# Optimization experiments

Hardware: AMD Instinct MI355X
Metric: run time of the kernel (lower is better)

## Reference

```python
import jax, jax.numpy as jnp
import numpy as np

N_NODES = 50000
N_EDGES = 800000
IN_CH = 128
OUT_CH = 64
HEADS = 2
NEG_SLOPE = 0.2


def _gat_conv(x, src, dst, W, a_src, a_dst, b, n):
    """PyG-style GATConv (eval mode: no dropout), self-loops already appended.
    x: [n, F_in]; W: [F_in, H*C]; a_src/a_dst: [H, C]; b: [H*C]."""
    H, C = a_src.shape
    h = (x @ W).reshape(n, H, C)                       # [n, H, C]
    alpha_src = jnp.sum(h * a_src, axis=-1)            # [n, H]
    alpha_dst = jnp.sum(h * a_dst, axis=-1)            # [n, H]
    e = alpha_src[src] + alpha_dst[dst]                # [E, H]
    e = jnp.where(e > 0, e, NEG_SLOPE * e)             # LeakyReLU(0.2)
    # neighbor-wise (destination-grouped) softmax, numerically stable
    m = jax.ops.segment_max(e, dst, num_segments=n)
    e = jnp.exp(e - m[dst])
    denom = jax.ops.segment_sum(e, dst, num_segments=n)
    alpha = e / (denom[dst] + 1e-16)                   # [E, H]
    out = jax.ops.segment_sum(alpha[:, :, None] * h[src], dst, num_segments=n)
    return out.reshape(n, H * C) + b


def setup_inputs() -> dict:
    key = jax.random.key(0)
    ks = jax.random.split(key, 12)
    s = 0.08  # glorot-ish scale
    x = jax.random.normal(ks[0], (N_NODES, IN_CH), dtype=jnp.float32)
    edge_index = jax.random.randint(ks[1], (2, N_EDGES), 0, N_NODES, dtype=jnp.int64)
    H, O = HEADS, OUT_CH
    return {
        "x": x,
        "edge_index": edge_index,
        "W1": jax.random.normal(ks[2], (IN_CH, H * 2 * O), dtype=jnp.float32) * s,
        "a_src1": jax.random.normal(ks[3], (H, 2 * O), dtype=jnp.float32) * s,
        "a_dst1": jax.random.normal(ks[4], (H, 2 * O), dtype=jnp.float32) * s,
        "b1": jnp.zeros((H * 2 * O,), dtype=jnp.float32),
        "W_mu": jax.random.normal(ks[5], (2 * O * H, H * O), dtype=jnp.float32) * s,
        "a_src_mu": jax.random.normal(ks[6], (H, O), dtype=jnp.float32) * s,
        "a_dst_mu": jax.random.normal(ks[7], (H, O), dtype=jnp.float32) * s,
        "b_mu": jnp.zeros((H * O,), dtype=jnp.float32),
        "W_ls": jax.random.normal(ks[8], (2 * O * H, H * O), dtype=jnp.float32) * s,
        "a_src_ls": jax.random.normal(ks[9], (H, O), dtype=jnp.float32) * s,
        "a_dst_ls": jax.random.normal(ks[10], (H, O), dtype=jnp.float32) * s,
        "b_ls": jnp.zeros((H * O,), dtype=jnp.float32),
    }


def reference(x, edge_index, W1, a_src1, a_dst1, b1,
              W_mu, a_src_mu, a_dst_mu, b_mu,
              W_ls, a_src_ls, a_dst_ls, b_ls):
    n = x.shape[0]
    loop = jnp.arange(n, dtype=edge_index.dtype)
    src = jnp.concatenate([edge_index[0], loop])  # PyG add_self_loops=True
    dst = jnp.concatenate([edge_index[1], loop])
    x1 = jax.nn.elu(_gat_conv(x, src, dst, W1, a_src1, a_dst1, b1, n))
    mu = _gat_conv(x1, src, dst, W_mu, a_src_mu, a_dst_mu, b_mu, n)
    logstd = _gat_conv(x1, src, dst, W_ls, a_src_ls, a_dst_ls, b_ls, n)
    return (mu, logstd)
```

## Files before the change

kernel.cpp:

```cpp
#include <hip/hip_runtime.h>


typedef unsigned short u16;
typedef unsigned int u32;
typedef _Float16 f16;
typedef f16 f16x8 __attribute__((ext_vector_type(8)));
typedef float f32x4v __attribute__((ext_vector_type(4)));

__device__ __forceinline__ u16 f2h(float f) {
    union { f16 h; u16 u; } t;
    t.h = (f16)f;
    return t.u;
}
__device__ __forceinline__ float4 loadh4(const u16* __restrict__ p, size_t i) {
    union { uint2 u; f16 h[4]; } t;
    t.u = *(const uint2*)(p + i);
    return make_float4((float)t.h[0], (float)t.h[1], (float)t.h[2], (float)t.h[3]);
}
__device__ __forceinline__ void store4(float* __restrict__ p, size_t i, float4 v) {
    *(float4*)(p + i) = v;
}
__device__ __forceinline__ void store4(u16* __restrict__ p, size_t i, float4 v) {
    union { uint2 u; f16 h[4]; } t;
    t.h[0] = (f16)v.x; t.h[1] = (f16)v.y; t.h[2] = (f16)v.z; t.h[3] = (f16)v.w;
    *(uint2*)(p + i) = t.u;
}

__global__ __launch_bounds__(256) void k_detect(const u32* __restrict__ ebuf,
                                                int* __restrict__ flag) {
    __shared__ int nz;
    if (threadIdx.x == 0) nz = 0;
    __syncthreads();
    if (ebuf[2 * threadIdx.x + 1] != 0u) atomicAdd(&nz, 1);
    __syncthreads();
    if (threadIdx.x == 0) *flag = (nz == 0) ? 1 : 0;
}

__global__ __launch_bounds__(256) void k_extract(const u32* __restrict__ ebuf, int E,
                                                 const int* __restrict__ flag,
                                                 int* __restrict__ se,
                                                 int* __restrict__ de,
                                                 int* __restrict__ deg) {
    int e = blockIdx.x * 256 + threadIdx.x;
    if (e >= E) return;
    int s, d;
    if (*flag) {
        s = (int)ebuf[2 * (size_t)e];
        d = (int)ebuf[2 * ((size_t)E + (size_t)e)];
    } else {
        s = (int)ebuf[e];
        d = (int)ebuf[(size_t)E + (size_t)e];
    }
    se[e] = s;
    de[e] = d;
    atomicAdd(&deg[d], 1);
}

__global__ __launch_bounds__(256) void k_scan_a(const int* __restrict__ deg, int n,
                                                int* __restrict__ bsum) {
    __shared__ int s[256];
    int i = blockIdx.x * 256 + threadIdx.x;
    s[threadIdx.x] = (i < n) ? deg[i] : 0;
    __syncthreads();
    for (int st = 128; st > 0; st >>= 1) {
        if (threadIdx.x < st) s[threadIdx.x] += s[threadIdx.x + st];
        __syncthreads();
    }
    if (threadIdx.x == 0) bsum[blockIdx.x] = s[0];
}

__global__ __launch_bounds__(256) void k_scan_b(int* __restrict__ bsum, int nb) {
    __shared__ int s[256];
    int t = threadIdx.x;
    int v = (t < nb) ? bsum[t] : 0;
    s[t] = v;
    __syncthreads();
    for (int off = 1; off < 256; off <<= 1) {
        int add = (t >= off) ? s[t - off] : 0;
        __syncthreads();
        s[t] += add;
        __syncthreads();
    }
    if (t < nb) bsum[t] = s[t] - v;
}

__global__ __launch_bounds__(256) void k_scan_c(const int* __restrict__ deg, int n,
                                                const int* __restrict__ bsum,
                                                int* __restrict__ rowptr,
                                                int* __restrict__ cursor, int E) {
    __shared__ int s[256];
    int t = threadIdx.x;
    int i = blockIdx.x * 256 + t;
    int v = (i < n) ? deg[i] : 0;
    s[t] = v;
    __syncthreads();
    for (int off = 1; off < 256; off <<= 1) {
        int add = (t >= off) ? s[t - off] : 0;
        __syncthreads();
        s[t] += add;
        __syncthreads();
    }
    if (i < n) {
        int ex = bsum[blockIdx.x] + s[t] - v;
        rowptr[i] = ex;
        cursor[i] = ex;
    }
    if (i == 0) rowptr[n] = E;
}

__global__ __launch_bounds__(256) void k_fill(const int* __restrict__ src,
                                              const int* __restrict__ dst, int E,
                                              int* __restrict__ cursor,
                                              int* __restrict__ csr_src,
                                              int* __restrict__ csr_dst) {
    int e = blockIdx.x * 256 + threadIdx.x;
    if (e < E) {
        int d = dst[e];
        int slot = atomicAdd(&cursor[d], 1);
        csr_src[slot] = src[e];
        csr_dst[slot] = d;
    }
}

__global__ __launch_bounds__(256) void k_tw(const float* __restrict__ Wl,
                                            const float* __restrict__ Wr, int split,
                                            int K, u16* __restrict__ Wt) {
    int idx = blockIdx.x * 256 + threadIdx.x;
    if (idx >= 256 * K) return;
    int c = idx / K, k = idx - c * K;
    float v;
    if (split == 256)
        v = Wl[(size_t)k * 256 + c];
    else
        v = (c < 128) ? Wl[(size_t)k * 128 + c] : Wr[(size_t)k * 128 + (c - 128)];
    Wt[idx] = f2h(v);
}

template <int NS>
__global__ __launch_bounds__(256) void k_w(const int* __restrict__ csr_src,
                                           const int* __restrict__ csr_dst,
                                           const float* __restrict__ as,
                                           const float* __restrict__ ad,
                                           float* __restrict__ wp, int E) {
    int i = blockIdx.x * 256 + threadIdx.x;
    if (i >= E) return;
    int s = csr_src[i], d = csr_dst[i];
    if (NS == 2) {
        float2 a = *(const float2*)(as + (size_t)s * 2);
        float2 b = *(const float2*)(ad + (size_t)d * 2);
        float e0 = a.x + b.x, e1 = a.y + b.y;
        e0 = fmaxf(e0, 0.2f * e0);
        e1 = fmaxf(e1, 0.2f * e1);
        wp[i] = __expf(e0);
        wp[(size_t)E + i] = __expf(e1);
    } else {
        float4 a = *(const float4*)(as + (size_t)s * 4);
        float4 b = *(const float4*)(ad + (size_t)d * 4);
        float e0 = a.x + b.x, e1 = a.y + b.y, e2 = a.z + b.z, e3 = a.w + b.w;
        e0 = fmaxf(e0, 0.2f * e0);
        e1 = fmaxf(e1, 0.2f * e1);
        e2 = fmaxf(e2, 0.2f * e2);
        e3 = fmaxf(e3, 0.2f * e3);
        wp[i] = __expf(e0);
        wp[(size_t)E + i] = __expf(e1);
        wp[2 * (size_t)E + i] = __expf(e2);
        wp[3 * (size_t)E + i] = __expf(e3);
    }
}

template <int K, int ALOGW, bool AF32>
__global__ __launch_bounds__(256) void k_gemm_mfma(
    const void* __restrict__ Av, const u16* __restrict__ Wt, u16* __restrict__ out,
    float* __restrict__ as_out, float* __restrict__ ad_out,
    const float* __restrict__ alo, const float* __restrict__ ahi,
    const float* __restrict__ dlo, const float* __restrict__ dhi, int M) {
    __shared__ u16 Bs[256 * 40];
    const int tid = threadIdx.x;
    const int wave = tid >> 6;
    const int lane = tid & 63;
    const int li = lane & 15;
    const int quad = lane >> 4;
    const int r0 = blockIdx.x * 128 + wave * 32;
    int ar0 = r0 + li;
    int ar1 = r0 + 16 + li;
    if (ar0 >= M) ar0 = M - 1;
    if (ar1 >= M) ar1 = M - 1;
    const u16* a16_0 = (const u16*)Av + (size_t)ar0 * K + quad * 8;
    const u16* a16_1 = (const u16*)Av + (size_t)ar1 * K + quad * 8;
    const float* a32_0 = (const float*)Av + (size_t)ar0 * K + quad * 8;
    const float* a32_1 = (const float*)Av + (size_t)ar1 * K + quad * 8;

    f32x4v acc0[16], acc1[16];
#pragma unroll
    for (int ct = 0; ct < 16; ct++) {
        acc0[ct] = (f32x4v)(0.f);
        acc1[ct] = (f32x4v)(0.f);
    }

    const u16* wrow = Wt + (size_t)tid * K;
    u16* dstp = Bs + tid * 40;
    uint4 sv0 = ((const uint4*)wrow)[0];
    uint4 sv1 = ((const uint4*)(wrow + 8))[0];
    uint4 sv2 = ((const uint4*)(wrow + 16))[0];
    uint4 sv3 = ((const uint4*)(wrow + 24))[0];
    uint4 p0a, p0b, p1a, p1b;
    if (AF32) {
        p0a = *(const uint4*)(a32_0);
        p0b = *(const uint4*)(a32_0 + 4);
        p1a = *(const uint4*)(a32_1);
        p1b = *(const uint4*)(a32_1 + 4);
    } else {
        p0a = *(const uint4*)(a16_0);
        p1a = *(const uint4*)(a16_1);
        p0b = p0a;
        p1b = p1a;
    }

    for (int t = 0; t < K; t += 32) {
        asm volatile("s_waitcnt lgkmcnt(0)" ::: "memory");
        __builtin_amdgcn_s_barrier();
        ((uint4*)dstp)[0] = sv0;
        ((uint4*)(dstp + 8))[0] = sv1;
        ((uint4*)(dstp + 16))[0] = sv2;
        ((uint4*)(dstp + 24))[0] = sv3;
        f16x8 a0, a1;
        if (AF32) {
            union { uint4 u; float f[4]; } ua, ub;
            ua.u = p0a; ub.u = p0b;
            a0[0] = (f16)ua.f[0]; a0[1] = (f16)ua.f[1];
            a0[2] = (f16)ua.f[2]; a0[3] = (f16)ua.f[3];
            a0[4] = (f16)ub.f[0]; a0[5] = (f16)ub.f[1];
            a0[6] = (f16)ub.f[2]; a0[7] = (f16)ub.f[3];
            ua.u = p1a; ub.u = p1b;
            a1[0] = (f16)ua.f[0]; a1[1] = (f16)ua.f[1];
            a1[2] = (f16)ua.f[2]; a1[3] = (f16)ua.f[3];
            a1[4] = (f16)ub.f[0]; a1[5] = (f16)ub.f[1];
            a1[6] = (f16)ub.f[2]; a1[7] = (f16)ub.f[3];
        } else {
            union { uint4 u; f16x8 h; } uh;
            uh.u = p0a; a0 = uh.h;
            uh.u = p1a; a1 = uh.h;
        }
        if (t + 32 < K) {
            const u16* s2 = wrow + t + 32;
            sv0 = ((const uint4*)s2)[0];
            sv1 = ((const uint4*)(s2 + 8))[0];
            sv2 = ((const uint4*)(s2 + 16))[0];
            sv3 = ((const uint4*)(s2 + 24))[0];
            if (AF32) {
                p0a = *(const uint4*)(a32_0 + t + 32);
                p0b = *(const uint4*)(a32_0 + t + 36);
                p1a = *(const uint4*)(a32_1 + t + 32);
                p1b = *(const uint4*)(a32_1 + t + 36);
            } else {
                p0a = *(const uint4*)(a16_0 + t + 32);
                p1a = *(const uint4*)(a16_1 + t + 32);
            }
        }
        asm volatile("s_waitcnt lgkmcnt(0)" ::: "memory");
        __builtin_amdgcn_s_barrier();
#pragma unroll
        for (int ct = 0; ct < 16; ct++) {
            f16x8 b = *(const f16x8*)(Bs + (ct * 16 + li) * 40 + quad * 8);
            acc0[ct] = __builtin_amdgcn_mfma_f32_16x16x32_f16(a0, b, acc0[ct], 0, 0, 0);
            acc1[ct] = __builtin_amdgcn_mfma_f32_16x16x32_f16(a1, b, acc1[ct], 0, 0, 0);
        }
    }

    const int NS = 64 >> ALOGW;
    const int SH = ALOGW - 2;
    float aw[16], dw[16];
#pragma unroll
    for (int ct = 0; ct < 16; ct++) {
        int col = ct * 16 + li;
        aw[ct] = (col < 128) ? alo[col] : ahi[col - 128];
        dw[ct] = (col < 128) ? dlo[col] : dhi[col - 128];
    }

    auto epilogue = [&](f32x4v(&acc)[16], int rbase) {
#pragma unroll
        for (int reg = 0; reg < 4; reg++) {
            int grow = rbase + quad * 4 + reg;
            if (grow < M) {
                u16* orow = out + (size_t)grow * 256 + li;
#pragma unroll
                for (int ct = 0; ct < 16; ct++) orow[ct * 16] = f2h(acc[ct][reg]);
            }
        }
#pragma unroll
        for (int reg = 0; reg < 4; reg++) {
            float s[4] = {0.f, 0.f, 0.f, 0.f};
            float d[4] = {0.f, 0.f, 0.f, 0.f};
#pragma unroll
            for (int ct = 0; ct < 16; ct++) {
                int sl = ct >> SH;
                s[sl] += acc[ct][reg] * aw[ct];
                d[sl] += acc[ct][reg] * dw[ct];
            }
#pragma unroll
            for (int sl = 0; sl < NS; sl++) {
#pragma unroll
                for (int m = 1; m <= 8; m <<= 1) {
                    s[sl] += __shfl_xor(s[sl], m, 64);
                    d[sl] += __shfl_xor(d[sl], m, 64);
                }
            }
            int grow = rbase + quad * 4 + reg;
            if (li == 0 && grow < M) {
#pragma unroll
                for (int sl = 0; sl < NS; sl++) {
                    as_out[(size_t)grow * NS + sl] = s[sl];
                    ad_out[(size_t)grow * NS + sl] = d[sl];
                }
            }
        }
    };
    epilogue(acc0, r0);
    epilogue(acc1, r0 + 16);
}

template <int LOGW, int MODE, typename OT>
__global__ __launch_bounds__(256) void k_agg4(
    const u16* __restrict__ h, const int* __restrict__ rowptr,
    const int* __restrict__ csr_src, const float* __restrict__ wp,
    const float* __restrict__ as, const float* __restrict__ ad,
    const float* __restrict__ b_lo, const float* __restrict__ b_hi,
    OT* __restrict__ outp, int n, int nGrp, int E) {
    const int NS = 64 >> LOGW;
    const int bid = blockIdx.x;
    const int xcd = bid & 7;
    const int half = xcd >> 2;
    const int grp = (bid >> 3) * 4 + (xcd & 3);
    if (grp >= nGrp) return;
    const int lane = threadIdx.x & 63;
    const int sub = lane >> 5;
    const int sl = lane & 31;
    const int wid0 = grp * 8 + (threadIdx.x >> 6) * 2 + sub;
    const bool ok = wid0 < n;
    const int wid = ok ? wid0 : (n - 1);
    const int col = half * 128 + sl * 4;
    const int slot = col >> (LOGW + 2);
    const float* __restrict__ wpl = wp + (size_t)slot * E;

    float e = as[(size_t)wid * NS + slot] + ad[(size_t)wid * NS + slot];
    e = fmaxf(e, 0.2f * e);
    float w = __expf(e);
    float denom = w;
    float4 hv = loadh4(h, (size_t)wid * 256 + col);
    float acc0 = w * hv.x, acc1 = w * hv.y, acc2 = w * hv.z, acc3 = w * hv.w;

    int rb = 0, re = 0;
    if (ok) { rb = rowptr[wid0]; re = rowptr[wid0 + 1]; }
    int p = rb;
    for (; p + 8 <= re; p += 8) {
        int4 sA = *(const int4*)(csr_src + p);
        int4 sB = *(const int4*)(csr_src + p + 4);
        float4 wA = *(const float4*)(wpl + p);
        float4 wB = *(const float4*)(wpl + p + 4);
        float4 h0 = loadh4(h, (size_t)sA.x * 256 + col);
        float4 h1 = loadh4(h, (size_t)sA.y * 256 + col);
        float4 h2 = loadh4(h, (size_t)sA.z * 256 + col);
        float4 h3 = loadh4(h, (size_t)sA.w * 256 + col);
        float4 h4 = loadh4(h, (size_t)sB.x * 256 + col);
        float4 h5 = loadh4(h, (size_t)sB.y * 256 + col);
        float4 h6 = loadh4(h, (size_t)sB.z * 256 + col);
        float4 h7 = loadh4(h, (size_t)sB.w * 256 + col);
        denom += (wA.x + wA.y + wA.z + wA.w) + (wB.x + wB.y + wB.z + wB.w);
        acc0 += wA.x * h0.x + wA.y * h1.x + wA.z * h2.x + wA.w * h3.x +
                wB.x * h4.x + wB.y * h5.x + wB.z * h6.x + wB.w * h7.x;
        acc1 += wA.x * h0.y + wA.y * h1.y + wA.z * h2.y + wA.w * h3.y +
                wB.x * h4.y + wB.y * h5.y + wB.z * h6.y + wB.w * h7.y;
        acc2 += wA.x * h0.z + wA.y * h1.z + wA.z * h2.z + wA.w * h3.z +
                wB.x * h4.z + wB.y * h5.z + wB.z * h6.z + wB.w * h7.z;
        acc3 += wA.x * h0.w + wA.y * h1.w + wA.z * h2.w + wA.w * h3.w +
                wB.x * h4.w + wB.y * h5.w + wB.z * h6.w + wB.w * h7.w;
    }
    for (; p + 4 <= re; p += 4) {
        int4 sA = *(const int4*)(csr_src + p);
        float4 wA = *(const float4*)(wpl + p);
        float4 h0 = loadh4(h, (size_t)sA.x * 256 + col);
        float4 h1 = loadh4(h, (size_t)sA.y * 256 + col);
        float4 h2 = loadh4(h, (size_t)sA.z * 256 + col);
        float4 h3 = loadh4(h, (size_t)sA.w * 256 + col);
        denom += (wA.x + wA.y) + (wA.z + wA.w);
        acc0 += wA.x * h0.x + wA.y * h1.x + wA.z * h2.x + wA.w * h3.x;
        acc1 += wA.x * h0.y + wA.y * h1.y + wA.z * h2.y + wA.w * h3.y;
        acc2 += wA.x * h0.z + wA.y * h1.z + wA.z * h2.z + wA.w * h3.z;
        acc3 += wA.x * h0.w + wA.y * h1.w + wA.z * h2.w + wA.w * h3.w;
    }
    for (; p < re; ++p) {
        int s = csr_src[p];
        float ww = wpl[p];
        float4 hh = loadh4(h, (size_t)s * 256 + col);
        denom += ww;
        acc0 += ww * hh.x;
        acc1 += ww * hh.y;
        acc2 += ww * hh.z;
        acc3 += ww * hh.w;
    }
    float inv = 1.0f / (denom + 1e-16f);

    const float* bp = half ? b_hi : b_lo;
    const int ci = sl * 4;
    float4 bv = *(const float4*)(bp + ci);
    float v0 = acc0 * inv + bv.x;
    float v1 = acc1 * inv + bv.y;
    float v2 = acc2 * inv + bv.z;
    float v3 = acc3 * inv + bv.w;

    if (!ok) return;
    if (MODE == 0) {
        v0 = v0 > 0.f ? v0 : expm1f(v0);
        v1 = v1 > 0.f ? v1 : expm1f(v1);
        v2 = v2 > 0.f ? v2 : expm1f(v2);
        v3 = v3 > 0.f ? v3 : expm1f(v3);
        store4((u16*)outp, (size_t)wid0 * 256 + col, make_float4(v0, v1, v2, v3));
    } else {
        size_t base = half ? ((size_t)n * 128 + (size_t)wid0 * 128 + ci)
                           : ((size_t)wid0 * 128 + ci);
        store4((float*)outp, base, make_float4(v0, v1, v2, v3));
    }
}

extern "C" void kernel_launch(void* const* d_in, const int* in_sizes, int n_in,
                              void* d_out, int out_size, void* d_ws, size_t ws_size,
                              hipStream_t stream) {
    const float* x = (const float*)d_in[0];
    const u32* ebuf = (const u32*)d_in[1];
    const float* W1 = (const float*)d_in[2];
    const float* a_src1 = (const float*)d_in[3];
    const float* a_dst1 = (const float*)d_in[4];
    const float* b1 = (const float*)d_in[5];
    const float* W_mu = (const float*)d_in[6];
    const float* a_src_mu = (const float*)d_in[7];
    const float* a_dst_mu = (const float*)d_in[8];
    const float* b_mu = (const float*)d_in[9];
    const float* W_ls = (const float*)d_in[10];
    const float* a_src_ls = (const float*)d_in[11];
    const float* a_dst_ls = (const float*)d_in[12];
    const float* b_ls = (const float*)d_in[13];

    const int n = in_sizes[0] / 128;
    const int E = in_sizes[1] / 2;

    char* base = (char*)d_ws;
    size_t off = 0;
    auto alloc = [&](size_t b) -> char* {
        char* p = base + off;
        off = (off + b + 255) & ~(size_t)255;
        return p;
    };
    int* rowptr = (int*)alloc((size_t)(n + 1) * 4);
    int* cursor = (int*)alloc((size_t)n * 4);
    int* csr = (int*)alloc((size_t)E * 4);
    int* csrd = (int*)alloc((size_t)E * 4);
    int* bsum = (int*)alloc(256 * 4);
    int* eflag = (int*)alloc(256);
    int* se = (int*)alloc((size_t)E * 4);
    int* de = (int*)alloc((size_t)E * 4);
    float* as = (float*)alloc((size_t)n * 4 * 4);
    float* ad = (float*)alloc((size_t)n * 4 * 4);
    float* wp = (float*)alloc((size_t)E * 4 * 4);
    u16* W1t = (u16*)alloc(256 * 128 * 2);
    u16* Wt2 = (u16*)alloc(256 * 256 * 2);
    u16* x1h = (u16*)alloc((size_t)n * 256 * 2);
    u16* h = (u16*)alloc((size_t)n * 256 * 2);

    const int nb = (n + 255) / 256;
    const int eg = (E + 255) / 256;
    const int gg = (n + 127) / 128;
    const int nGrp = (n + 7) / 8;
    const int aggGrid = 8 * ((nGrp + 3) / 4);

    hipMemsetAsync(cursor, 0, (size_t)n * 4, stream);
    k_detect<<<1, 256, 0, stream>>>(ebuf, eflag);
    k_extract<<<eg, 256, 0, stream>>>(ebuf, E, eflag, se, de, cursor);
    k_scan_a<<<nb, 256, 0, stream>>>(cursor, n, bsum);
    k_scan_b<<<1, 256, 0, stream>>>(bsum, nb);
    k_scan_c<<<nb, 256, 0, stream>>>(cursor, n, bsum, rowptr, cursor, E);
    k_fill<<<eg, 256, 0, stream>>>(se, de, E, cursor, csr, csrd);

    k_tw<<<(256 * 128 + 255) / 256, 256, 0, stream>>>(W1, W1, 256, 128, W1t);
    k_tw<<<(256 * 256 + 255) / 256, 256, 0, stream>>>(W_mu, W_ls, 128, 256, Wt2);

    k_gemm_mfma<128, 5, true><<<gg, 256, 0, stream>>>(x, W1t, h, as, ad, a_src1,
                                                      a_src1 + 128, a_dst1,
                                                      a_dst1 + 128, n);
    k_w<2><<<eg, 256, 0, stream>>>(csr, csrd, as, ad, wp, E);
    k_agg4<5, 0, u16><<<aggGrid, 256, 0, stream>>>(h, rowptr, csr, wp, as, ad, b1,
                                                   b1 + 128, x1h, n, nGrp, E);

    k_gemm_mfma<256, 4, false><<<gg, 256, 0, stream>>>(x1h, Wt2, h, as, ad,
                                                       a_src_mu, a_src_ls,
                                                       a_dst_mu, a_dst_ls, n);
    k_w<4><<<eg, 256, 0, stream>>>(csr, csrd, as, ad, wp, E);
    k_agg4<4, 1, float><<<aggGrid, 256, 0, stream>>>(h, rowptr, csr, wp, as, ad,
                                                     b_mu, b_ls, (float*)d_out, n,
                                                     nGrp, E);
}
```

Measured before the change: 388.4 us.

## Aggregate raw features before layer-1 GEMM and precompute attention vectors

Layer 1 now uses linearity: attention logits come from x·(W·a) vectors computed up front, and neighbour aggregation runs on the 128-wide fp16 input features (per head) before the GEMM with W1. The layer-1 GEMM then applies bias and ELU and produces the layer-2 attention scores from precomputed W_mu/W_ls·a vectors. The separate detect kernel is folded into extract, and edge arrays are padded. The aim is to gather narrower rows in the first aggregation and shrink epilogue work. The cost is a few extra small kernels and a different rounding order for the fp16 aggregates.

After: 432.2 us. 11.3% more time.

```diff
diff --git a/kernel.cpp b/kernel.cpp
--- a/kernel.cpp
+++ b/kernel.cpp
@@ -20,31 +20,26 @@
 __device__ __forceinline__ void store4(float* __restrict__ p, size_t i, float4 v) {
     *(float4*)(p + i) = v;
 }
-__device__ __forceinline__ void store4(u16* __restrict__ p, size_t i, float4 v) {
+__device__ __forceinline__ void store4h(u16* __restrict__ p, size_t i, float4 v) {
     union { uint2 u; f16 h[4]; } t;
     t.h[0] = (f16)v.x; t.h[1] = (f16)v.y; t.h[2] = (f16)v.z; t.h[3] = (f16)v.w;
     *(uint2*)(p + i) = t.u;
 }
 
-__global__ __launch_bounds__(256) void k_detect(const u32* __restrict__ ebuf,
-                                                int* __restrict__ flag) {
+__global__ __launch_bounds__(256) void k_extract(const u32* __restrict__ ebuf, int E,
+                                                 int* __restrict__ se,
+                                                 int* __restrict__ de,
+                                                 int* __restrict__ deg) {
     __shared__ int nz;
     if (threadIdx.x == 0) nz = 0;
     __syncthreads();
     if (ebuf[2 * threadIdx.x + 1] != 0u) atomicAdd(&nz, 1);
     __syncthreads();
-    if (threadIdx.x == 0) *flag = (nz == 0) ? 1 : 0;
-}
-
-__global__ __launch_bounds__(256) void k_extract(const u32* __restrict__ ebuf, int E,
-                                                 const int* __restrict__ flag,
-                                                 int* __restrict__ se,
-                                                 int* __restrict__ de,
-                                                 int* __restrict__ deg) {
+    const bool i64 = (nz == 0);
     int e = blockIdx.x * 256 + threadIdx.x;
     if (e >= E) return;
     int s, d;
-    if (*flag) {
+    if (i64) {
         s = (int)ebuf[2 * (size_t)e];
         d = (int)ebuf[2 * ((size_t)E + (size_t)e)];
     } else {
@@ -114,6 +109,7 @@
                                               int* __restrict__ csr_src,
                                               int* __restrict__ csr_dst) {
     int e = blockIdx.x * 256 + threadIdx.x;
+    if (e < 8) csr_src[E + e] = 0;
     if (e < E) {
         int d = dst[e];
         int slot = atomicAdd(&cursor[d], 1);
@@ -136,12 +132,89 @@
     Wt[idx] = f2h(v);
 }
 
+__global__ void k_vdots1(const float* __restrict__ W1,
+                         const float* __restrict__ a_src,
+                         const float* __restrict__ a_dst,
+                         float* __restrict__ v1) {
+    int c = threadIdx.x;
+    if (c >= 128) return;
+    const float* wr = W1 + (size_t)c * 256;
+    float s0 = 0, s1 = 0, d0 = 0, d1 = 0;
+    for (int j = 0; j < 128; j++) {
+        float w0 = wr[j], w1 = wr[128 + j];
+        s0 += w0 * a_src[j];
+        s1 += w1 * a_src[128 + j];
+        d0 += w0 * a_dst[j];
+        d1 += w1 * a_dst[128 + j];
+    }
+    v1[c] = s0;
+    v1[128 + c] = s1;
+    v1[256 + c] = d0;
+    v1[384 + c] = d1;
+}
+
+__global__ void k_vdots2(const float* __restrict__ Wmu, const float* __restrict__ Wls,
+                         const float* __restrict__ smu, const float* __restrict__ dmu,
+                         const float* __restrict__ sls, const float* __restrict__ dls,
+                         float* __restrict__ v2s, float* __restrict__ v2d) {
+    int j = threadIdx.x;
+    const float* wm = Wmu + (size_t)j * 128;
+    const float* wl = Wls + (size_t)j * 128;
+    float s0 = 0, s1 = 0, s2 = 0, s3 = 0, d0 = 0, d1 = 0, d2 = 0, d3 = 0;
+    for (int k = 0; k < 64; k++) {
+        float m0 = wm[k], m1 = wm[64 + k], l0 = wl[k], l1 = wl[64 + k];
+        s0 += m0 * smu[k];
+        s1 += m1 * smu[64 + k];
+        s2 += l0 * sls[k];
+        s3 += l1 * sls[64 + k];
+        d0 += m0 * dmu[k];
+        d1 += m1 * dmu[64 + k];
+        d2 += l0 * dls[k];
+        d3 += l1 * dls[64 + k];
+    }
+    v2s[j] = s0; v2s[256 + j] = s1; v2s[512 + j] = s2; v2s[768 + j] = s3;
+    v2d[j] = d0; v2d[256 + j] = d1; v2d[512 + j] = d2; v2d[768 + j] = d3;
+}
+
+__global__ __launch_bounds__(256) void k_cvt_asad(const float* __restrict__ x,
+                                                  const float* __restrict__ v1,
+                                                  u16* __restrict__ xh,
+                                                  float* __restrict__ as,
+                                                  float* __restrict__ ad, int n) {
+    int wid = blockIdx.x * 4 + (threadIdx.x >> 6);
+    if (wid >= n) return;
+    int lane = threadIdx.x & 63;
+    float2 xv = *(const float2*)(x + (size_t)wid * 128 + lane * 2);
+    union { u32 u; f16 h[2]; } t;
+    t.h[0] = (f16)xv.x;
+    t.h[1] = (f16)xv.y;
+    *(u32*)(xh + (size_t)wid * 128 + lane * 2) = t.u;
+    int c = lane * 2;
+    float s0 = xv.x * v1[c] + xv.y * v1[c + 1];
+    float s1 = xv.x * v1[128 + c] + xv.y * v1[128 + c + 1];
+    float d0 = xv.x * v1[256 + c] + xv.y * v1[256 + c + 1];
+    float d1 = xv.x * v1[384 + c] + xv.y * v1[384 + c + 1];
+#pragma unroll
+    for (int m = 1; m <= 32; m <<= 1) {
+        s0 += __shfl_xor(s0, m, 64);
+        s1 += __shfl_xor(s1, m, 64);
+        d0 += __shfl_xor(d0, m, 64);
+        d1 += __shfl_xor(d1, m, 64);
+    }
+    if (lane == 0) {
+        as[(size_t)wid * 2] = s0;
+        as[(size_t)wid * 2 + 1] = s1;
+        ad[(size_t)wid * 2] = d0;
+        ad[(size_t)wid * 2 + 1] = d1;
+    }
+}
+
 template <int NS>
 __global__ __launch_bounds__(256) void k_w(const int* __restrict__ csr_src,
                                            const int* __restrict__ csr_dst,
                                            const float* __restrict__ as,
                                            const float* __restrict__ ad,
-                                           float* __restrict__ wp, int E) {
+                                           float* __restrict__ wp, int E, int Ep) {
     int i = blockIdx.x * 256 + threadIdx.x;
     if (i >= E) return;
     int s = csr_src[i], d = csr_dst[i];
@@ -152,7 +225,7 @@
         e0 = fmaxf(e0, 0.2f * e0);
         e1 = fmaxf(e1, 0.2f * e1);
         wp[i] = __expf(e0);
-        wp[(size_t)E + i] = __expf(e1);
+        wp[(size_t)Ep + i] = __expf(e1);
     } else {
         float4 a = *(const float4*)(as + (size_t)s * 4);
         float4 b = *(const float4*)(ad + (size_t)d * 4);
@@ -162,18 +235,116 @@
         e2 = fmaxf(e2, 0.2f * e2);
         e3 = fmaxf(e3, 0.2f * e3);
         wp[i] = __expf(e0);
-        wp[(size_t)E + i] = __expf(e1);
-        wp[2 * (size_t)E + i] = __expf(e2);
-        wp[3 * (size_t)E + i] = __expf(e3);
-    }
-}
-
-template <int K, int ALOGW, bool AF32>
-__global__ __launch_bounds__(256) void k_gemm_mfma(
-    const void* __restrict__ Av, const u16* __restrict__ Wt, u16* __restrict__ out,
+        wp[(size_t)Ep + i] = __expf(e1);
+        wp[2 * (size_t)Ep + i] = __expf(e2);
+        wp[3 * (size_t)Ep + i] = __expf(e3);
+    }
+}
+
+__global__ __launch_bounds__(256) void k_agg1(
+    const u16* __restrict__ xh, const int* __restrict__ rowptr,
+    const int* __restrict__ csr_src, const float* __restrict__ wp,
+    const float* __restrict__ as, const float* __restrict__ ad,
+    u16* __restrict__ aggout, int n, int Ep) {
+    const int lane = threadIdx.x & 63;
+    const int sub = lane >> 5;
+    const int sl = lane & 31;
+    const int wid0 = blockIdx.x * 8 + (threadIdx.x >> 6) * 2 + sub;
+    const bool ok = wid0 < n;
+    const int wid = ok ? wid0 : (n - 1);
+    const int col = sl * 4;
+    const float* __restrict__ wp0 = wp;
+    const float* __restrict__ wp1 = wp + Ep;
+
+    float e0 = as[(size_t)wid * 2] + ad[(size_t)wid * 2];
+    float e1 = as[(size_t)wid * 2 + 1] + ad[(size_t)wid * 2 + 1];
+    e0 = fmaxf(e0, 0.2f * e0);
+    e1 = fmaxf(e1, 0.2f * e1);
+    float w0s = __expf(e0), w1s = __expf(e1);
+    float den0 = w0s, den1 = w1s;
+    float4 hv = loadh4(xh, (size_t)wid * 128 + col);
+    float a0x = w0s * hv.x, a0y = w0s * hv.y, a0z = w0s * hv.z, a0w = w0s * hv.w;
+    float b0x = w1s * hv.x, b0y = w1s * hv.y, b0z = w1s * hv.z, b0w = w1s * hv.w;
+
+    int rb = 0, re = 0;
+    if (ok) { rb = rowptr[wid0]; re = rowptr[wid0 + 1]; }
+    int p = rb;
+    for (; p + 8 <= re; p += 8) {
+        int4 sA = *(const int4*)(csr_src + p);
+        int4 sB = *(const int4*)(csr_src + p + 4);
+        float4 uA = *(const float4*)(wp0 + p);
+        float4 uB = *(const float4*)(wp0 + p + 4);
+        float4 vA = *(const float4*)(wp1 + p);
+        float4 vB = *(const float4*)(wp1 + p + 4);
+        float4 h0 = loadh4(xh, (size_t)sA.x * 128 + col);
+        float4 h1 = loadh4(xh, (size_t)sA.y * 128 + col);
+        float4 h2 = loadh4(xh, (size_t)sA.z * 128 + col);
+        float4 h3 = loadh4(xh, (size_t)sA.w * 128 + col);
+        float4 h4 = loadh4(xh, (size_t)sB.x * 128 + col);
+        float4 h5 = loadh4(xh, (size_t)sB.y * 128 + col);
+        float4 h6 = loadh4(xh, (size_t)sB.z * 128 + col);
+        float4 h7 = loadh4(xh, (size_t)sB.w * 128 + col);
+        den0 += (uA.x + uA.y + uA.z + uA.w) + (uB.x + uB.y + uB.z + uB.w);
+        den1 += (vA.x + vA.y + vA.z + vA.w) + (vB.x + vB.y + vB.z + vB.w);
+        a0x += uA.x * h0.x + uA.y * h1.x + uA.z * h2.x + uA.w * h3.x +
+               uB.x * h4.x + uB.y * h5.x + uB.z * h6.x + uB.w * h7.x;
+        a0y += uA.x * h0.y + uA.y * h1.y + uA.z * h2.y + uA.w * h3.y +
+               uB.x * h4.y + uB.y * h5.y + uB.z * h6.y + uB.w * h7.y;
+        a0z += uA.x * h0.z + uA.y * h1.z + uA.z * h2.z + uA.w * h3.z +
+               uB.x * h4.z + uB.y * h5.z + uB.z * h6.z + uB.w * h7.z;
+        a0w += uA.x * h0.w + uA.y * h1.w + uA.z * h2.w + uA.w * h3.w +
+               uB.x * h4.w + uB.y * h5.w + uB.z * h6.w + uB.w * h7.w;
+        b0x += vA.x * h0.x + vA.y * h1.x + vA.z * h2.x + vA.w * h3.x +
+               vB.x * h4.x + vB.y * h5.x + vB.z * h6.x + vB.w * h7.x;
+        b0y += vA.x * h0.y + vA.y * h1.y + vA.z * h2.y + vA.w * h3.y +
+               vB.x * h4.y + vB.y * h5.y + vB.z * h6.y + vB.w * h7.y;
+        b0z += vA.x * h0.z + vA.y * h1.z + vA.z * h2.z + vA.w * h3.z +
+               vB.x * h4.z + vB.y * h5.z + vB.z * h6.z + vB.w * h7.z;
+        b0w += vA.x * h0.w + vA.y * h1.w + vA.z * h2.w + vA.w * h3.w +
+               vB.x * h4.w + vB.y * h5.w + vB.z * h6.w + vB.w * h7.w;
+    }
+    for (; p + 4 <= re; p += 4) {
+        int4 sA = *(const int4*)(csr_src + p);
+        float4 uA = *(const float4*)(wp0 + p);
+        float4 vA = *(const float4*)(wp1 + p);
+        float4 h0 = loadh4(xh, (size_t)sA.x * 128 + col);
+        float4 h1 = loadh4(xh, (size_t)sA.y * 128 + col);
+        float4 h2 = loadh4(xh, (size_t)sA.z * 128 + col);
+        float4 h3 = loadh4(xh, (size_t)sA.w * 128 + col);
+        den0 += (uA.x + uA.y) + (uA.z + uA.w);
+        den1 += (vA.x + vA.y) + (vA.z + vA.w);
+        a0x += uA.x * h0.x + uA.y * h1.x + uA.z * h2.x + uA.w * h3.x;
+        a0y += uA.x * h0.y + uA.y * h1.y + uA.z * h2.y + uA.w * h3.y;
+        a0z += uA.x * h0.z + uA.y * h1.z + uA.z * h2.z + uA.w * h3.z;
+        a0w += uA.x * h0.w + uA.y * h1.w + uA.z * h2.w + uA.w * h3.w;
+        b0x += vA.x * h0.x + vA.y * h1.x + vA.z * h2.x + vA.w * h3.x;
+        b0y += vA.x * h0.y + vA.y * h1.y + vA.z * h2.y + vA.w * h3.y;
+        b0z += vA.x * h0.z + vA.y * h1.z + vA.z * h2.z + vA.w * h3.z;
+        b0w += vA.x * h0.w + vA.y * h1.w + vA.z * h2.w + vA.w * h3.w;
+    }
+    for (; p < re; ++p) {
+        int s = csr_src[p];
+        float u = wp0[p], v = wp1[p];
+        float4 hh = loadh4(xh, (size_t)s * 128 + col);
+        den0 += u;
+        den1 += v;
+        a0x += u * hh.x; a0y += u * hh.y; a0z += u * hh.z; a0w += u * hh.w;
+        b0x += v * hh.x; b0y += v * hh.y; b0z += v * hh.z; b0w += v * hh.w;
+    }
+    if (!ok) return;
+    float i0 = 1.0f / (den0 + 1e-16f);
+    float i1 = 1.0f / (den1 + 1e-16f);
+    store4h(aggout, (size_t)wid0 * 256 + col,
+            make_float4(a0x * i0, a0y * i0, a0z * i0, a0w * i0));
+    store4h(aggout, (size_t)wid0 * 256 + 128 + col,
+            make_float4(b0x * i1, b0y * i1, b0z * i1, b0w * i1));
+}
+
+__global__ __launch_bounds__(256) void k_gemm_x1(
+    const u16* __restrict__ Ag, const u16* __restrict__ Wt, u16* __restrict__ x1out,
     float* __restrict__ as_out, float* __restrict__ ad_out,
-    const float* __restrict__ alo, const float* __restrict__ ahi,
-    const float* __restrict__ dlo, const float* __restrict__ dhi, int M) {
+    const float* __restrict__ b1, const float* __restrict__ v2s,
+    const float* __restrict__ v2d, int M) {
     __shared__ u16 Bs[256 * 40];
     const int tid = threadIdx.x;
     const int wave = tid >> 6;
@@ -185,10 +356,10 @@
     int ar1 = r0 + 16 + li;
     if (ar0 >= M) ar0 = M - 1;
     if (ar1 >= M) ar1 = M - 1;
-    const u16* a16_0 = (const u16*)Av + (size_t)ar0 * K + quad * 8;
-    const u16* a16_1 = (const u16*)Av + (size_t)ar1 * K + quad * 8;
-    const float* a32_0 = (const float*)Av + (size_t)ar0 * K + quad * 8;
-    const float* a32_1 = (const float*)Av + (size_t)ar1 * K + quad * 8;
+    const u16* a00p = Ag + (size_t)ar0 * 256 + quad * 8;
+    const u16* a01p = Ag + (size_t)ar0 * 256 + 128 + quad * 8;
+    const u16* a10p = Ag + (size_t)ar1 * 256 + quad * 8;
+    const u16* a11p = Ag + (size_t)ar1 * 256 + 128 + quad * 8;
 
     f32x4v acc0[16], acc1[16];
 #pragma unroll
@@ -197,65 +368,163 @@
         acc1[ct] = (f32x4v)(0.f);
     }
 
-    const u16* wrow = Wt + (size_t)tid * K;
+    const u16* wrow = Wt + (size_t)tid * 128;
     u16* dstp = Bs + tid * 40;
     uint4 sv0 = ((const uint4*)wrow)[0];
     uint4 sv1 = ((const uint4*)(wrow + 8))[0];
     uint4 sv2 = ((const uint4*)(wrow + 16))[0];
     uint4 sv3 = ((const uint4*)(wrow + 24))[0];
-    uint4 p0a, p0b, p1a, p1b;
-    if (AF32) {
-        p0a = *(const uint4*)(a32_0);
-        p0b = *(const uint4*)(a32_0 + 4);
-        p1a = *(const uint4*)(a32_1);
-        p1b = *(const uint4*)(a32_1 + 4);
-    } else {
-        p0a = *(const uint4*)(a16_0);
-        p1a = *(const uint4*)(a16_1);
-        p0b = p0a;
-        p1b = p1a;
-    }
-
-    for (int t = 0; t < K; t += 32) {
+    uint4 p00 = *(const uint4*)a00p;
+    uint4 p01 = *(const uint4*)a01p;
+    uint4 p10 = *(const uint4*)a10p;
+    uint4 p11 = *(const uint4*)a11p;
+
+    for (int t = 0; t < 128; t += 32) {
         asm volatile("s_waitcnt lgkmcnt(0)" ::: "memory");
         __builtin_amdgcn_s_barrier();
         ((uint4*)dstp)[0] = sv0;
         ((uint4*)(dstp + 8))[0] = sv1;
         ((uint4*)(dstp + 16))[0] = sv2;
         ((uint4*)(dstp + 24))[0] = sv3;
-        f16x8 a0, a1;
-        if (AF32) {
-            union { uint4 u; float f[4]; } ua, ub;
-            ua.u = p0a; ub.u = p0b;
-            a0[0] = (f16)ua.f[0]; a0[1] = (f16)ua.f[1];
-            a0[2] = (f16)ua.f[2]; a0[3] = (f16)ua.f[3];
-            a0[4] = (f16)ub.f[0]; a0[5] = (f16)ub.f[1];
-            a0[6] = (f16)ub.f[2]; a0[7] = (f16)ub.f[3];
-            ua.u = p1a; ub.u = p1b;
-            a1[0] = (f16)ua.f[0]; a1[1] = (f16)ua.f[1];
-            a1[2] = (f16)ua.f[2]; a1[3] = (f16)ua.f[3];
-            a1[4] = (f16)ub.f[0]; a1[5] = (f16)ub.f[1];
-            a1[6] = (f16)ub.f[2]; a1[7] = (f16)ub.f[3];
-        } else {
-            union { uint4 u; f16x8 h; } uh;
-            uh.u = p0a; a0 = uh.h;
-            uh.u = p1a; a1 = uh.h;
-        }
-        if (t + 32 < K) {
+        union { uint4 u; f16x8 h; } uh;
+        f16x8 a00, a01, a10, a11;
+        uh.u = p00; a00 = uh.h;
+        uh.u = p01; a01 = uh.h;
+        uh.u = p10; a10 = uh.h;
+        uh.u = p11; a11 = uh.h;
+        if (t + 32 < 128) {
             const u16* s2 = wrow + t + 32;
             sv0 = ((const uint4*)s2)[0];
             sv1 = ((const uint4*)(s2 + 8))[0];
             sv2 = ((const uint4*)(s2 + 16))[0];
             sv3 = ((const uint4*)(s2 + 24))[0];
-            if (AF32) {
-                p0a = *(const uint4*)(a32_0 + t + 32);
-                p0b = *(const uint4*)(a32_0 + t + 36);
-                p1a = *(const uint4*)(a32_1 + t + 32);
-                p1b = *(const uint4*)(a32_1 + t + 36);
+            p00 = *(const uint4*)(a00p + t + 32);
+            p01 = *(const uint4*)(a01p + t + 32);
+            p10 = *(const uint4*)(a10p + t + 32);
+            p11 = *(const uint4*)(a11p + t + 32);
+        }
+        asm volatile("s_waitcnt lgkmcnt(0)" ::: "memory");
+        __builtin_amdgcn_s_barrier();
+#pragma unroll
+        for (int ct = 0; ct < 16; ct++) {
+            f16x8 b = *(const f16x8*)(Bs + (ct * 16 + li) * 40 + quad * 8);
+            if (ct < 8) {
+                acc0[ct] = __builtin_amdgcn_mfma_f32_16x16x32_f16(a00, b, acc0[ct], 0, 0, 0);
+                acc1[ct] = __builtin_amdgcn_mfma_f32_16x16x32_f16(a10, b, acc1[ct], 0, 0, 0);
             } else {
-                p0a = *(const uint4*)(a16_0 + t + 32);
-                p1a = *(const uint4*)(a16_1 + t + 32);
+                acc0[ct] = __builtin_amdgcn_mfma_f32_16x16x32_f16(a01, b, acc0[ct], 0, 0, 0);
+                acc1[ct] = __builtin_amdgcn_mfma_f32_16x16x32_f16(a11, b, acc1[ct], 0, 0, 0);
             }
+        }
+    }
+
+    float bval[16];
+#pragma unroll
+    for (int ct = 0; ct < 16; ct++) bval[ct] = b1[ct * 16 + li];
+
+    auto epilogue = [&](f32x4v(&acc)[16], int rbase) {
+#pragma unroll
+        for (int ct = 0; ct < 16; ct++) {
+#pragma unroll
+            for (int reg = 0; reg < 4; reg++) {
+                float v = acc[ct][reg] + bval[ct];
+                acc[ct][reg] = v > 0.f ? v : expm1f(v);
+            }
+        }
+#pragma unroll
+        for (int reg = 0; reg < 4; reg++) {
+            int grow = rbase + quad * 4 + reg;
+            if (grow < M) {
+                u16* orow = x1out + (size_t)grow * 256 + li;
+#pragma unroll
+                for (int ct = 0; ct < 16; ct++) orow[ct * 16] = f2h(acc[ct][reg]);
+            }
+        }
+#pragma unroll
+        for (int sl = 0; sl < 4; sl++) {
+            float aw[16], dw[16];
+#pragma unroll
+            for (int ct = 0; ct < 16; ct++) {
+                aw[ct] = v2s[sl * 256 + ct * 16 + li];
+                dw[ct] = v2d[sl * 256 + ct * 16 + li];
+            }
+#pragma unroll
+            for (int reg = 0; reg < 4; reg++) {
+                float s = 0.f, d = 0.f;
+#pragma unroll
+                for (int ct = 0; ct < 16; ct++) {
+                    s += acc[ct][reg] * aw[ct];
+                    d += acc[ct][reg] * dw[ct];
+                }
+#pragma unroll
+                for (int m = 1; m <= 8; m <<= 1) {
+                    s += __shfl_xor(s, m, 64);
+                    d += __shfl_xor(d, m, 64);
+                }
+                int grow = rbase + quad * 4 + reg;
+                if (li == 0 && grow < M) {
+                    as_out[(size_t)grow * 4 + sl] = s;
+                    ad_out[(size_t)grow * 4 + sl] = d;
+                }
+            }
+        }
+    };
+    epilogue(acc0, r0);
+    epilogue(acc1, r0 + 16);
+}
+
+__global__ __launch_bounds__(256) void k_gemm_h(const u16* __restrict__ Ah,
+                                                const u16* __restrict__ Wt,
+                                                u16* __restrict__ out, int M) {
+    __shared__ u16 Bs[256 * 40];
+    const int tid = threadIdx.x;
+    const int wave = tid >> 6;
+    const int lane = tid & 63;
+    const int li = lane & 15;
+    const int quad = lane >> 4;
+    const int r0 = blockIdx.x * 128 + wave * 32;
+    int ar0 = r0 + li;
+    int ar1 = r0 + 16 + li;
+    if (ar0 >= M) ar0 = M - 1;
+    if (ar1 >= M) ar1 = M - 1;
+    const u16* a0p = Ah + (size_t)ar0 * 256 + quad * 8;
+    const u16* a1p = Ah + (size_t)ar1 * 256 + quad * 8;
+
+    f32x4v acc0[16], acc1[16];
+#pragma unroll
+    for (int ct = 0; ct < 16; ct++) {
+        acc0[ct] = (f32x4v)(0.f);
+        acc1[ct] = (f32x4v)(0.f);
+    }
+
+    const u16* wrow = Wt + (size_t)tid * 256;
+    u16* dstp = Bs + tid * 40;
+    uint4 sv0 = ((const uint4*)wrow)[0];
+    uint4 sv1 = ((const uint4*)(wrow + 8))[0];
+    uint4 sv2 = ((const uint4*)(wrow + 16))[0];
+    uint4 sv3 = ((const uint4*)(wrow + 24))[0];
+    uint4 p0 = *(const uint4*)a0p;
+    uint4 p1 = *(const uint4*)a1p;
+
+    for (int t = 0; t < 256; t += 32) {
+        asm volatile("s_waitcnt lgkmcnt(0)" ::: "memory");
+        __builtin_amdgcn_s_barrier();
+        ((uint4*)dstp)[0] = sv0;
+        ((uint4*)(dstp + 8))[0] = sv1;
+        ((uint4*)(dstp + 16))[0] = sv2;
+        ((uint4*)(dstp + 24))[0] = sv3;
+        union { uint4 u; f16x8 h; } uh;
+        f16x8 a0, a1;
+        uh.u = p0; a0 = uh.h;
+        uh.u = p1; a1 = uh.h;
+        if (t + 32 < 256) {
+            const u16* s2 = wrow + t + 32;
+            sv0 = ((const uint4*)s2)[0];
+            sv1 = ((const uint4*)(s2 + 8))[0];
+            sv2 = ((const uint4*)(s2 + 16))[0];
+            sv3 = ((const uint4*)(s2 + 24))[0];
+            p0 = *(const uint4*)(a0p + t + 32);
+            p1 = *(const uint4*)(a1p + t + 32);
         }
         asm volatile("s_waitcnt lgkmcnt(0)" ::: "memory");
         __builtin_amdgcn_s_barrier();
@@ -266,67 +535,30 @@
             acc1[ct] = __builtin_amdgcn_mfma_f32_16x16x32_f16(a1, b, acc1[ct], 0, 0, 0);
         }
     }
-
-    const int NS = 64 >> ALOGW;
-    const int SH = ALOGW - 2;
-    float aw[16], dw[16];
-#pragma unroll
-    for (int ct = 0; ct < 16; ct++) {
-        int col = ct * 16 + li;
-        aw[ct] = (col < 128) ? alo[col] : ahi[col - 128];
-        dw[ct] = (col < 128) ? dlo[col] : dhi[col - 128];
-    }
-
-    auto epilogue = [&](f32x4v(&acc)[16], int rbase) {
-#pragma unroll
-        for (int reg = 0; reg < 4; reg++) {
-            int grow = rbase + quad * 4 + reg;
-            if (grow < M) {
-                u16* orow = out + (size_t)grow * 256 + li;
-#pragma unroll
-                for (int ct = 0; ct < 16; ct++) orow[ct * 16] = f2h(acc[ct][reg]);
-            }
-        }
-#pragma unroll
-        for (int reg = 0; reg < 4; reg++) {
-            float s[4] = {0.f, 0.f, 0.f, 0.f};
-            float d[4] = {0.f, 0.f, 0.f, 0.f};
-#pragma unroll
-            for (int ct = 0; ct < 16; ct++) {
-                int sl = ct >> SH;
-                s[sl] += acc[ct][reg] * aw[ct];
-                d[sl] += acc[ct][reg] * dw[ct];
-            }
-#pragma unroll
-            for (int sl = 0; sl < NS; sl++) {
-#pragma unroll
-                for (int m = 1; m <= 8; m <<= 1) {
-                    s[sl] += __shfl_xor(s[sl], m, 64);
-                    d[sl] += __shfl_xor(d[sl], m, 64);
-                }
-            }
-            int grow = rbase + quad * 4 + reg;
-            if (li == 0 && grow < M) {
-#pragma unroll
-                for (int sl = 0; sl < NS; sl++) {
-                    as_out[(size_t)grow * NS + sl] = s[sl];
-                    ad_out[(size_t)grow * NS + sl] = d[sl];
-                }
-            }
-        }
-    };
-    epilogue(acc0, r0);
-    epilogue(acc1, r0 + 16);
-}
-
-template <int LOGW, int MODE, typename OT>
+#pragma unroll
+    for (int reg = 0; reg < 4; reg++) {
+        int g0 = r0 + quad * 4 + reg;
+        if (g0 < M) {
+            u16* orow = out + (size_t)g0 * 256 + li;
+#pragma unroll
+            for (int ct = 0; ct < 16; ct++) orow[ct * 16] = f2h(acc0[ct][reg]);
+        }
+        int g1 = r0 + 16 + quad * 4 + reg;
+        if (g1 < M) {
+            u16* orow = out + (size_t)g1 * 256 + li;
+#pragma unroll
+            for (int ct = 0; ct < 16; ct++) orow[ct * 16] = f2h(acc1[ct][reg]);
+        }
+    }
+}
+
 __global__ __launch_bounds__(256) void k_agg4(
     const u16* __restrict__ h, const int* __restrict__ rowptr,
     const int* __restrict__ csr_src, const float* __restrict__ wp,
     const float* __restrict__ as, const float* __restrict__ ad,
     const float* __restrict__ b_lo, const float* __restrict__ b_hi,
-    OT* __restrict__ outp, int n, int nGrp, int E) {
-    const int NS = 64 >> LOGW;
+    float* __restrict__ outp, int n, int nGrp, int Ep) {
+    const int NS = 4;
     const int bid = blockIdx.x;
     const int xcd = bid & 7;
     const int half = xcd >> 2;
@@ -339,8 +571,8 @@
     const bool ok = wid0 < n;
     const int wid = ok ? wid0 : (n - 1);
     const int col = half * 128 + sl * 4;
-    const int slot = col >> (LOGW + 2);
-    const float* __restrict__ wpl = wp + (size_t)slot * E;
+    const int slot = col >> 6;
+    const float* __restrict__ wpl = wp + (size_t)slot * Ep;
 
     float e = as[(size_t)wid * NS + slot] + ad[(size_t)wid * NS + slot];
     e = fmaxf(e, 0.2f * e);
@@ -409,17 +641,9 @@
     float v3 = acc3 * inv + bv.w;
 
     if (!ok) return;
-    if (MODE == 0) {
-        v0 = v0 > 0.f ? v0 : expm1f(v0);
-        v1 = v1 > 0.f ? v1 : expm1f(v1);
-        v2 = v2 > 0.f ? v2 : expm1f(v2);
-        v3 = v3 > 0.f ? v3 : expm1f(v3);
-        store4((u16*)outp, (size_t)wid0 * 256 + col, make_float4(v0, v1, v2, v3));
-    } else {
-        size_t base = half ? ((size_t)n * 128 + (size_t)wid0 * 128 + ci)
-                           : ((size_t)wid0 * 128 + ci);
-        store4((float*)outp, base, make_float4(v0, v1, v2, v3));
-    }
+    size_t base = half ? ((size_t)n * 128 + (size_t)wid0 * 128 + ci)
+                       : ((size_t)wid0 * 128 + ci);
+    store4(outp, base, make_float4(v0, v1, v2, v3));
 }
 
 extern "C" void kernel_launch(void* const* d_in, const int* in_sizes, int n_in,
@@ -442,6 +666,7 @@
 
     const int n = in_sizes[0] / 128;
     const int E = in_sizes[1] / 2;
+    const int Ep = E + 8;
 
     char* base = (char*)d_ws;
     size_t off = 0;
@@ -452,29 +677,32 @@
     };
     int* rowptr = (int*)alloc((size_t)(n + 1) * 4);
     int* cursor = (int*)alloc((size_t)n * 4);
-    int* csr = (int*)alloc((size_t)E * 4);
+    int* csr = (int*)alloc((size_t)Ep * 4);
     int* csrd = (int*)alloc((size_t)E * 4);
     int* bsum = (int*)alloc(256 * 4);
-    int* eflag = (int*)alloc(256);
     int* se = (int*)alloc((size_t)E * 4);
     int* de = (int*)alloc((size_t)E * 4);
     float* as = (float*)alloc((size_t)n * 4 * 4);
     float* ad = (float*)alloc((size_t)n * 4 * 4);
-    float* wp = (float*)alloc((size_t)E * 4 * 4);
+    float* wp = (float*)alloc((size_t)Ep * 4 * 4);
+    float* v1 = (float*)alloc(4 * 128 * 4);
+    float* v2s = (float*)alloc(4 * 256 * 4);
+    float* v2d = (float*)alloc(4 * 256 * 4);
     u16* W1t = (u16*)alloc(256 * 128 * 2);
     u16* Wt2 = (u16*)alloc(256 * 256 * 2);
     u16* x1h = (u16*)alloc((size_t)n * 256 * 2);
+    u16* xh = x1h;
     u16* h = (u16*)alloc((size_t)n * 256 * 2);
+    u16* aggx = h;
 
     const int nb = (n + 255) / 256;
     const int eg = (E + 255) / 256;
     const int gg = (n + 127) / 128;
     const int nGrp = (n + 7) / 8;
-    const int aggGrid = 8 * ((nGrp + 3) / 4);
+    const int aggGrid2 = 8 * ((nGrp + 3) / 4);
 
     hipMemsetAsync(cursor, 0, (size_t)n * 4, stream);
-    k_detect<<<1, 256, 0, stream>>>(ebuf, eflag);
-    k_extract<<<eg, 256, 0, stream>>>(ebuf, E, eflag, se, de, cursor);
+    k_extract<<<eg, 256, 0, stream>>>(ebuf, E, se, de, cursor);
     k_scan_a<<<nb, 256, 0, stream>>>(cursor, n, bsum);
     k_scan_b<<<1, 256, 0, stream>>>(bsum, nb);
     k_scan_c<<<nb, 256, 0, stream>>>(cursor, n, bsum, rowptr, cursor, E);
@@ -482,19 +710,17 @@
 
     k_tw<<<(256 * 128 + 255) / 256, 256, 0, stream>>>(W1, W1, 256, 128, W1t);
     k_tw<<<(256 * 256 + 255) / 256, 256, 0, stream>>>(W_mu, W_ls, 128, 256, Wt2);
-
-    k_gemm_mfma<128, 5, true><<<gg, 256, 0, stream>>>(x, W1t, h, as, ad, a_src1,
-                                                      a_src1 + 128, a_dst1,
-                                                      a_dst1 + 128, n);
-    k_w<2><<<eg, 256, 0, stream>>>(csr, csrd, as, ad, wp, E);
-    k_agg4<5, 0, u16><<<aggGrid, 256, 0, stream>>>(h, rowptr, csr, wp, as, ad, b1,
-                                                   b1 + 128, x1h, n, nGrp, E);
-
-    k_gemm_mfma<256, 4, false><<<gg, 256, 0, stream>>>(x1h, Wt2, h, as, ad,
-                                                       a_src_mu, a_src_ls,
-                                                       a_dst_mu, a_dst_ls, n);
-    k_w<4><<<eg, 256, 0, stream>>>(csr, csrd, as, ad, wp, E);
-    k_agg4<4, 1, float><<<aggGrid, 256, 0, stream>>>(h, rowptr, csr, wp, as, ad,
-                                                     b_mu, b_ls, (float*)d_out, n,
-                                                     nGrp, E);
-}
+    k_vdots1<<<1, 128, 0, stream>>>(W1, a_src1, a_dst1, v1);
+    k_vdots2<<<1, 256, 0, stream>>>(W_mu, W_ls, a_src_mu, a_dst_mu, a_src_ls,
+                                    a_dst_ls, v2s, v2d);
+    k_cvt_asad<<<(n + 3) / 4, 256, 0, stream>>>(x, v1, xh, as, ad, n);
+
+    k_w<2><<<eg, 256, 0, stream>>>(csr, csrd, as, ad, wp, E, Ep);
+    k_agg1<<<(n + 7) / 8, 256, 0, stream>>>(xh, rowptr, csr, wp, as, ad, aggx, n, Ep);
+    k_gemm_x1<<<gg, 256, 0, stream>>>(aggx, W1t, x1h, as, ad, b1, v2s, v2d, n);
+
+    k_w<4><<<eg, 256, 0, stream>>>(csr, csrd, as, ad, wp, E, Ep);
+    k_gemm_h<<<gg, 256, 0, stream>>>(x1h, Wt2, h, n);
+    k_agg4<<<aggGrid2, 256, 0, stream>>>(h, rowptr, csr, wp, as, ad, b_mu, b_ls,
+                                         (float*)d_out, n, nGrp, Ep);
+}
```
